# Optimization experiments

Measured on AMD Instinct MI355X. Metric: run time of the kernel, lower is better.

The kernel has to match this reference:

```python
import jax, jax.numpy as jnp
import numpy as np


def conv2d(x, w, pad):
    # x: [N,C,H,W], w: [O,I,kh,kw]
    return jax.lax.conv_general_dilated(
        x, w, window_strides=(1, 1), padding=[(pad, pad), (pad, pad)],
        dimension_numbers=("NCHW", "OIHW", "NCHW"))


def group_norm1(x, g, b, eps=1e-5):
    # GroupNorm(1, C): normalize over (C,H,W) per sample, per-channel affine
    mu = jnp.mean(x, axis=(1, 2, 3), keepdims=True)
    var = jnp.mean((x - mu) ** 2, axis=(1, 2, 3), keepdims=True)
    xn = (x - mu) * jax.lax.rsqrt(var + eps)
    return xn * g[None, :, None, None] + b[None, :, None, None]


def maxpool_3x3_s2(x):
    return jax.lax.reduce_window(
        x, -jnp.inf, jax.lax.max, (1, 1, 3, 3), (1, 1, 2, 2),
        ((0, 0), (0, 0), (1, 1), (1, 1)))


def hr2o_layer(x, wq, wk, wv, wo, g, b):
    # x: [N,C,H,W]; pairwise attention over the N ROIs at each (h,w)
    q = conv2d(x, wq, 1)
    k = conv2d(x, wk, 1)
    v = conv2d(x, wv, 1)
    scale = 1.0 / jnp.sqrt(jnp.asarray(x.shape[1], x.dtype))
    # torch: (q.unsqueeze(1) * k.unsqueeze(0)).sum(2) == einsum over channels
    att = jnp.einsum("nchw,mchw->nmhw", q, k) * scale  # [N,N,H,W]
    att = jax.nn.softmax(att, axis=1)                    # softmax over keys (dim=1)
    virt = jnp.einsum("nmhw,mchw->nchw", att, v)        # [N,C,H,W]
    virt = jax.nn.relu(group_norm1(virt, g, b))
    virt = conv2d(virt, wo, 1)
    return x + virt  # dropout is identity in eval mode


def setup_inputs() -> dict:
    key = jax.random.key(0)
    ks = jax.random.split(key, 12)
    N, C_R, H, W, HID, NCLS, DEPTH = 64, 1024, 16, 16, 512, 60, 2
    s = 0.02
    return {
        "bg_feats": jax.random.normal(ks[0], (C_R, H, W), jnp.float32),
        "actor_feats": jax.random.normal(ks[1], (N, C_R), jnp.float32),
        "w_conv1": jax.random.normal(ks[2], (HID, 2 * C_R, 1, 1), jnp.float32) * s,
        "w_conv2": jax.random.normal(ks[3], (HID, HID, 3, 3), jnp.float32) * s,
        "w_q": jax.random.normal(ks[4], (DEPTH, HID, HID, 3, 3), jnp.float32) * s,
        "w_k": jax.random.normal(ks[5], (DEPTH, HID, HID, 3, 3), jnp.float32) * s,
        "w_v": jax.random.normal(ks[6], (DEPTH, HID, HID, 3, 3), jnp.float32) * s,
        "w_o": jax.random.normal(ks[7], (DEPTH, HID, HID, 3, 3), jnp.float32) * s,
        "gamma": jnp.ones((DEPTH, HID), jnp.float32),
        "beta": jnp.zeros((DEPTH, HID), jnp.float32),
        "w_fc1": jax.random.normal(ks[8], (HID, C_R), jnp.float32) * s,
        "w_fc2": jax.random.normal(ks[9], (NCLS, 2 * HID), jnp.float32) * s,
    }


def reference(bg_feats, actor_feats, w_conv1, w_conv2, w_q, w_k, w_v, w_o,
              gamma, beta, w_fc1, w_fc2):
    N = actor_feats.shape[0]
    C_R, H, W = bg_feats.shape
    # bg repeated per ROI, actor features tiled over spatial dims
    bg = jnp.broadcast_to(bg_feats[None], (N, C_R, H, W))
    tiled = jnp.broadcast_to(actor_feats[:, :, None, None], (N, C_R, H, W))
    x = jnp.concatenate([bg, tiled], axis=1)           # [N, 2*C_R, H, W]
    x = jax.nn.relu(conv2d(x, w_conv1, 0))             # 1x1 -> [N,HID,H,W]
    x = jax.nn.relu(conv2d(x, w_conv2, 0))             # 3x3 pad=0 -> H-2,W-2
    x = maxpool_3x3_s2(x)                              # -> 7x7
    for d in range(w_q.shape[0]):
        x = hr2o_layer(x, w_q[d], w_k[d], w_v[d], w_o[d], gamma[d], beta[d])
    high_order = jnp.mean(x, axis=(2, 3))              # gap -> [N,HID]
    roi = jax.nn.relu(actor_feats @ w_fc1.T)           # [N,HID]
    out = jnp.concatenate([roi, high_order], axis=1) @ w_fc2.T  # [N,num_classes]
    return out
```

## Files before the change

### kernel.cpp

```cpp
#include <hip/hip_runtime.h>
#include <math.h>


typedef __bf16 bf16x8 __attribute__((ext_vector_type(8)));
typedef float  f32x4  __attribute__((ext_vector_type(4)));

#define NROI 64
#define CR   1024
#define HIDC 512
#define NCLS 60
#define PLANE (NROI * HIDC * 49)
#define ROWH 40
#define OCALL 4608
#define TAPSTR ((size_t)OCALL * 512)
#define WL (HIDC * HIDC * 9)
#define GNCNT 25088.0f

#if defined(__has_builtin)
#  if __has_builtin(__builtin_amdgcn_global_load_lds)
#    define HAVE_GLL 1
#  endif
#endif

__device__ __forceinline__ void stage16(const void* g, void* lds_base, int lane) {
#ifdef HAVE_GLL
    __builtin_amdgcn_global_load_lds(
        (const __attribute__((address_space(1))) unsigned int*)g,
        (__attribute__((address_space(3))) unsigned int*)lds_base, 16, 0, 0);
#else
    *(uint4*)((char*)lds_base + lane * 16) = *(const uint4*)g;
#endif
}

__device__ __forceinline__ float bf2f(unsigned short h) {
    union { unsigned u; float f; } x; x.u = (unsigned)h << 16; return x.f;
}

__device__ __forceinline__ unsigned short f2bfu(float f) {
    return __builtin_bit_cast(unsigned short, (__bf16)f);
}

__device__ __forceinline__ int swzkey(int r) {
    return (r & 3) ^ ((r >> 2) & 3);
}

__global__ __launch_bounds__(256) void k_mega(
    const float* __restrict__ bg, const float* __restrict__ actor,
    const float* __restrict__ w1, const float* __restrict__ wfc1,
    const float* __restrict__ w2, const float* __restrict__ wq,
    const float* __restrict__ wk, const float* __restrict__ wv,
    const float* __restrict__ wo,
    float* __restrict__ A_T, float* __restrict__ Bp, float* __restrict__ roi,
    __bf16* __restrict__ wAll, __bf16* __restrict__ inT7)
{
    const int b = blockIdx.x, tid = threadIdx.x;
    __shared__ __align__(16) char smem[18432];

    if (b < 48) {
        const int bx = b % 6, by = b / 6;
        const bool isA = bx < 4;
        const bool isRoi = (bx == 5);
        const int ocWg = by * 64;
        const int w = tid >> 6, lane = tid & 63;
        const int q = lane >> 4, l16 = lane & 15;
        __bf16* s_a = (__bf16*)smem;
        __bf16* s_b = s_a + 64 * ROWH;

        f32x4 acc[4];
#pragma unroll
        for (int nt = 0; nt < 4; ++nt) acc[nt] = (f32x4){0.f, 0.f, 0.f, 0.f};

        const int row = tid >> 2, part = tid & 3;
        for (int ch = 0; ch < 32; ++ch) {
            const int c0 = ch * 32;
            __syncthreads();
            if (isA) {
                const int gp = bx * 64 + row;
                bf16x8 val;
#pragma unroll
                for (int j = 0; j < 8; ++j)
                    val[j] = (__bf16)bg[(size_t)(c0 + part * 8 + j) * 256 + gp];
                *(bf16x8*)(&s_a[row * ROWH + part * 8]) = val;
            } else {
                const float* src = actor + (size_t)row * CR + c0 + part * 8;
                bf16x8 val;
#pragma unroll
                for (int j = 0; j < 8; ++j) val[j] = (__bf16)src[j];
                *(bf16x8*)(&s_a[row * ROWH + part * 8]) = val;
            }
            {
                const float* srcb = isRoi
                    ? (wfc1 + (size_t)(ocWg + row) * CR + c0 + part * 8)
                    : (w1 + (size_t)(ocWg + row) * (2 * CR)
                          + (isA ? 0 : CR) + c0 + part * 8);
                bf16x8 vb;
#pragma unroll
                for (int j = 0; j < 8; ++j) vb[j] = (__bf16)srcb[j];
                *(bf16x8*)(&s_b[row * ROWH + part * 8]) = vb;
            }
            __syncthreads();
            const bf16x8 af = *(const bf16x8*)(&s_a[(w * 16 + l16) * ROWH + q * 8]);
#pragma unroll
            for (int nt = 0; nt < 4; ++nt) {
                const bf16x8 bw = *(const bf16x8*)(&s_b[(nt * 16 + l16) * ROWH + q * 8]);
                acc[nt] = __builtin_amdgcn_mfma_f32_16x16x32_bf16(af, bw, acc[nt], 0, 0, 0);
            }
        }
#pragma unroll
        for (int r = 0; r < 4; ++r) {
#pragma unroll
            for (int nt = 0; nt < 4; ++nt) {
                const int mrow = w * 16 + q * 4 + r;
                const int oc = ocWg + nt * 16 + l16;
                if (isA)       A_T[(size_t)(bx * 64 + mrow) * 512 + oc] = acc[nt][r];
                else if (isRoi) roi[(size_t)mrow * 512 + oc] = fmaxf(acc[nt][r], 0.f);
                else           Bp[(size_t)mrow * 512 + oc] = acc[nt][r];
            }
        }
    } else if (b < 4656) {
        const int bid = b - 48;
        const float* src;
        if (bid < 512) src = w2 + (size_t)bid * 4608;
        else if (bid < 2048) {
            const int r = bid - 512;
            const float* bb = r < 512 ? wq : (r < 1024 ? wk : wv);
            src = bb + (size_t)(r & 511) * 4608;
        } else if (bid < 2560) src = wo + (size_t)(bid - 2048) * 4608;
        else if (bid < 4096) {
            const int r = bid - 2560;
            const float* bb = r < 512 ? wq : (r < 1024 ? wk : wv);
            src = bb + WL + (size_t)(r & 511) * 4608;
        } else src = wo + WL + (size_t)(bid - 4096) * 4608;
        float* s = (float*)smem;
        const float4* s4 = (const float4*)src;
        for (int i = tid; i < 1152; i += 256) ((float4*)s)[i] = s4[i];
        __syncthreads();
        for (int u = tid; u < 576; u += 256) {
            const int t = u / 64, o = u - (u / 64) * 64;
            const int swz = (o & 3) ^ ((bid >> 1) & 3);
            const int cbase = o * 8;
            unsigned pack[4];
#pragma unroll
            for (int h = 0; h < 4; ++h) {
                const unsigned short lo = f2bfu(s[(cbase + 2 * h) * 9 + t]);
                const unsigned short hi = f2bfu(s[(cbase + 2 * h + 1) * 9 + t]);
                pack[h] = ((unsigned)hi << 16) | lo;
            }
            const size_t cidx = (size_t)(o >> 2) * 32 + (size_t)swz * 8;
            *(uint4*)(wAll + (size_t)t * TAPSTR + (size_t)bid * 512 + cidx) =
                *(const uint4*)pack;
        }
    } else {
        const int k = b - 4656;
        const int n = k >> 3;
        const int j0 = (k & 7) * 4;
#pragma unroll
        for (int i = 0; i < 4; ++i) {
            const int jj = j0 + i;
            int sp;
            if (jj < 9) sp = jj;
            else if (jj < 18) sp = 63 + jj;
            else { const int t = jj - 18; sp = (1 + (t >> 1)) * 9 + (t & 1) * 8; }
            unsigned* d = (unsigned*)(inT7 + ((size_t)n * 81 + sp) * 512);
            d[tid] = 0u;
        }
    }
}

__global__ __launch_bounds__(256) void k_prep_in2(
    const float* __restrict__ A_T, const float* __restrict__ B,
    __bf16* __restrict__ dst)
{
    const int vn = blockIdx.x;
    const int n = vn >> 2, quad = vn & 3;
    const int sp0 = blockIdx.y * 27;
    const float b0 = B[n * HIDC + threadIdx.x];
    const float b1 = B[n * HIDC + 256 + threadIdx.x];
    for (int sp = sp0; sp < sp0 + 27; ++sp) {
        const int r = sp / 9, w = sp % 9;
        const int p16 = ((quad >> 1) * 7 + r) * 16 + (quad & 1) * 7 + w;
        __bf16* d = dst + ((size_t)vn * 81 + sp) * 512;
        d[threadIdx.x]       = (__bf16)fmaxf(A_T[p16 * HIDC + threadIdx.x] + b0, 0.f);
        d[256 + threadIdx.x] = (__bf16)fmaxf(A_T[p16 * HIDC + 256 + threadIdx.x] + b1, 0.f);
    }
}

__global__ __launch_bounds__(256) void k_prep_gn(
    const float* __restrict__ virt, const float* __restrict__ statsRaw,
    const float* __restrict__ gamma, const float* __restrict__ beta,
    __bf16* __restrict__ gnT)
{
    const int vn = blockIdx.x;
    const int sp0 = blockIdx.y * 9;
    __shared__ float s_mi[2];
    if (threadIdx.x == 0) {
        const float S = statsRaw[vn * 2], Q = statsRaw[vn * 2 + 1];
        const float mean = S / GNCNT;
        s_mi[0] = mean;
        s_mi[1] = rsqrtf(Q / GNCNT - mean * mean + 1e-5f);
    }
    __syncthreads();
    const float m = s_mi[0], iv = s_mi[1];
    const int c0 = threadIdx.x, c1 = threadIdx.x + 256;
    const float g0 = gamma[c0], g1 = gamma[c1];
    const float b0 = beta[c0],  b1 = beta[c1];
    for (int sp = sp0; sp < sp0 + 9; ++sp) {
        const int rr = sp / 9, cc = sp % 9;
        __bf16* d = gnT + ((size_t)vn * 81 + sp) * 512;
        if (rr >= 1 && rr <= 7 && cc >= 1 && cc <= 7) {
            const int p = (rr - 1) * 7 + (cc - 1);
            const float* src = virt + ((size_t)vn * 49 + p) * 512;
            d[c0] = (__bf16)fmaxf((src[c0] - m) * iv * g0 + b0, 0.f);
            d[c1] = (__bf16)fmaxf((src[c1] - m) * iv * g1 + b1, 0.f);
        } else {
            d[c0] = (__bf16)0.f;
            d[c1] = (__bf16)0.f;
        }
    }
}

template<int VN, int MODE, int OCT>
__global__ __launch_bounds__(256, (VN == 4) ? 2 : 3) void k_conv_pipe(
    const __bf16* __restrict__ inT,
    const __bf16* __restrict__ wAll, int ocBaseGl,
    __bf16* __restrict__ outb,
    float* __restrict__ zeroStats, float* __restrict__ gapZero,
    const float* __restrict__ resid, float* __restrict__ outf,
    __bf16* __restrict__ inT7out, float* __restrict__ gapOut)
{
    constexpr int MT = (VN == 4) ? 4 : 2;
    constexpr int SLOTS = VN * 324;
    constexpr int NSUB = (SLOTS + 255) / 256;
    constexpr int SBUF = NSUB * 256;
    constexpr int NI = NSUB / 3;
    constexpr int WTAP = OCT * 512;
    constexpr int SWSZ = 2 * 3 * WTAP + ((OCT == 2) ? 1024 : 0);
    const int tid = threadIdx.x;
    const int w = tid >> 6, lane = tid & 63;
    const int q = lane >> 4, l16 = lane & 15;
    const int vn_l = (VN == 4) ? w : (w & 1);
    const int mh   = (VN == 4) ? 0 : (w >> 1);
    const int vnBase = blockIdx.x * VN;
    const int ocWg = blockIdx.y * (OCT * 16);

    if (zeroStats && blockIdx.x == 0 && blockIdx.y == 0 && tid < 128)
        zeroStats[tid] = 0.f;
    if (gapZero && blockIdx.y == 0 && blockIdx.x < 16) {
        const float4 z = {0.f, 0.f, 0.f, 0.f};
        ((float4*)gapZero)[blockIdx.x * 512 + tid * 2]     = z;
        ((float4*)gapZero)[blockIdx.x * 512 + tid * 2 + 1] = z;
    }

    __shared__ __align__(16) __bf16 s_w[SWSZ];
    __shared__ __align__(16) __bf16 s_in[2 * SBUF * 8];

    unsigned iGo[NSUB];
#pragma unroll
    for (int s = 0; s < NSUB; ++s) {
        int idx = tid + s * 256;
        if (idx > SLOTS - 1) idx = SLOTS - 1;
        const int vnl = idx / 324, rem = idx - vnl * 324;
        const int r = rem >> 2, part = rem & 3;
        iGo[s] = (unsigned)(((vnBase + vnl) * 81 + r) * 512
                            + ((part ^ swzkey(r)) * 8));
    }
    unsigned wGo4 = 0;
    unsigned wGo2[2]; int wJ2[2];
    if constexpr (OCT == 4) {
        wGo4 = (unsigned)((ocBaseGl + ocWg + (tid >> 2)) * 512 + (tid & 3) * 8);
    } else {
#pragma unroll
        for (int k = 0; k < 2; ++k) {
            const int u = tid + k * 256;
            const int jj = (u >> 7) > 2 ? 2 : (u >> 7);
            const int row = (u >> 2) & 31, part = u & 3;
            wGo2[k] = (unsigned)((ocBaseGl + ocWg + row) * 512 + part * 8);
            wJ2[k] = jj;
        }
    }
    const int bOff = l16 * 32 + ((q ^ ((l16 >> 1) & 3)) << 3);

    int aLoc[MT];
#pragma unroll
    for (int mt = 0; mt < MT; ++mt) {
        int p = (mh * MT + mt) * 16 + l16;
        p = p > 48 ? 48 : p;
        aLoc[mt] = (p / 7) * 9 + (p % 7);
    }
    const int vb81 = vn_l * 81;

    f32x4 acc[MT][OCT];
#pragma unroll
    for (int a = 0; a < MT; ++a)
#pragma unroll
        for (int b = 0; b < OCT; ++b) acc[a][b] = (f32x4){0.f, 0.f, 0.f, 0.f};

    auto stageW = [&](int fn, int cc, int wparN) {
        if constexpr (OCT == 4) {
#pragma unroll
            for (int j = 0; j < 3; ++j)
                stage16(wAll + (size_t)(fn * 3 + j) * TAPSTR + wGo4 + cc,
                        (char*)s_w + (size_t)(wparN * 3 + j) * (WTAP * 2)
                                    + (size_t)w * 1024, lane);
        } else {
#pragma unroll
            for (int k = 0; k < 2; ++k) {
                const int ubase = (tid & ~63) + k * 256;
                char* dst;
                if (ubase < 384)
                    dst = (char*)s_w
                        + (size_t)(wparN * 3 + (ubase >> 7)) * (WTAP * 2)
                        + (size_t)(ubase & 127) * 16;
                else
                    dst = (char*)s_w + (size_t)(2 * 3 * WTAP) * 2
                        + (size_t)(ubase - 384) * 16;
                stage16(wAll + (size_t)(fn * 3 + wJ2[k]) * TAPSTR + wGo2[k] + cc,
                        dst, lane);
            }
        }
    };

#pragma unroll
    for (int s = 0; s < NSUB; ++s)
        stage16(inT + iGo[s],
                (char*)s_in + (size_t)(s * 256 + w * 64) * 16, lane);
    stageW(0, 0, 0);
    __syncthreads();

    for (int ch = 0; ch < 16; ++ch) {
        const int c0 = ch * 32;
        const int cur = ch & 1;
        const int nxt = cur ^ 1;
#pragma unroll
        for (int f = 0; f < 3; ++f) {
            const int P = ch * 3 + f;
            const int wpar = P & 1;
            {
                const int fn = (f == 2) ? 0 : (f + 1);
                const int cc = (f == 2) ? (c0 + 32) : c0;
                stageW(fn, cc, wpar ^ 1);
            }
#pragma unroll
            for (int u = 0; u < NI; ++u) {
                const int s = f * NI + u;
                stage16(inT + iGo[s] + c0 + 32,
                        (char*)s_in + (size_t)nxt * (SBUF * 16)
                                    + (size_t)(s * 256 + w * 64) * 16, lane);
            }
            if (f == 0) {
                if constexpr (OCT == 4) {
                    if constexpr (NI == 2) asm volatile("s_waitcnt vmcnt(5)" ::: "memory");
                    else                   asm volatile("s_waitcnt vmcnt(4)" ::: "memory");
                } else {
                    asm volatile("s_waitcnt vmcnt(3)" ::: "memory");
                }
            } else {
                if constexpr (OCT == 4) {
                    if constexpr (NI == 2) asm volatile("s_waitcnt vmcnt(7)" ::: "memory");
                    else                   asm volatile("s_waitcnt vmcnt(5)" ::: "memory");
                } else {
                    asm volatile("s_waitcnt vmcnt(4)" ::: "memory");
                }
            }
            __builtin_amdgcn_sched_barrier(0);
            __builtin_amdgcn_s_barrier();
            __builtin_amdgcn_sched_barrier(0);
#pragma unroll
            for (int j = 0; j < 3; ++j) {
                const int DT = f * 9 + j;
                bf16x8 bw[OCT];
#pragma unroll
                for (int nt = 0; nt < OCT; ++nt)
                    bw[nt] = *(const bf16x8*)(
                        &s_w[(wpar * 3 + j) * WTAP + nt * 512 + bOff]);
                bf16x8 af[MT];
#pragma unroll
                for (int mt = 0; mt < MT; ++mt) {
                    const int rl = aLoc[mt] + DT;
                    const int col = (q ^ swzkey(rl)) << 3;
                    af[mt] = *(const bf16x8*)(
                        &s_in[cur * (SBUF * 8) + (vb81 + rl) * 32 + col]);
                }
#pragma unroll
                for (int mt = 0; mt < MT; ++mt)
#pragma unroll
                    for (int nt = 0; nt < OCT; ++nt)
                        acc[mt][nt] = __builtin_amdgcn_mfma_f32_16x16x32_bf16(
                            af[mt], bw[nt], acc[mt][nt], 0, 0, 0);
            }
            __builtin_amdgcn_sched_barrier(0);
            __builtin_amdgcn_s_barrier();
        }
    }

    const int vn = vnBase + vn_l;
    float gsum[OCT];
#pragma unroll
    for (int nt = 0; nt < OCT; ++nt) gsum[nt] = 0.f;
#pragma unroll
    for (int mt = 0; mt < MT; ++mt) {
#pragma unroll
        for (int r = 0; r < 4; ++r) {
            const int p = (mh * MT + mt) * 16 + q * 4 + r;
            if (p >= 49) continue;
#pragma unroll
            for (int nt = 0; nt < OCT; ++nt) {
                const int oc = ocWg + nt * 16 + l16;
                const float v = acc[mt][nt][r];
                if constexpr (MODE == 2) {
                    const int n = vn >> 2, quad = vn & 3;
                    const int p14 = ((quad >> 1) * 7 + p / 7) * 14 + (quad & 1) * 7 + p % 7;
                    outb[((size_t)n * 196 + p14) * 512 + oc] = (__bf16)fmaxf(v, 0.f);
                } else if constexpr (MODE == 1) {
                    const size_t addr = ((size_t)vn * 49 + p) * 512 + oc;
                    const float res = v + resid[addr];
                    if (!gapOut) outf[addr] = res;
                    gsum[nt] += res;
                    if (inT7out) {
                        const int sp = (p / 7 + 1) * 9 + (p % 7 + 1);
                        inT7out[((size_t)vn * 81 + sp) * 512 + oc] = (__bf16)res;
                    }
                } else {
                    const int conv = oc >> 9;
                    outb[(size_t)conv * PLANE + ((size_t)p * 64 + vn) * 512 + (oc & 511)]
                        = (__bf16)v;
                }
            }
        }
    }
    if constexpr (MODE == 1) {
        if (gapOut) {
#pragma unroll
            for (int nt = 0; nt < OCT; ++nt)
                atomicAdd(gapOut + (size_t)vn * 512 + ocWg + nt * 16 + l16, gsum[nt]);
        }
    }
}

__global__ __launch_bounds__(256) void k_pool_prep(
    const __bf16* __restrict__ x2, __bf16* __restrict__ inT7,
    float* __restrict__ xA)
{
    const int b = blockIdx.x;
    const int n = b / 49, p = b % 49;
    const int i = p / 7, j = p % 7;
    const int sp = (i + 1) * 9 + (j + 1);
#pragma unroll
    for (int k = 0; k < 2; ++k) {
        const int c = threadIdx.x + k * 256;
        float mx = -1e30f;
#pragma unroll
        for (int di = -1; di <= 1; ++di) {
            const int rr = 2 * i + di;
            if (rr < 0 || rr >= 14) continue;
#pragma unroll
            for (int dj = -1; dj <= 1; ++dj) {
                const int cc = 2 * j + dj;
                if (cc < 0 || cc >= 14) continue;
                mx = fmaxf(mx, (float)x2[((size_t)n * 196 + rr * 14 + cc) * 512 + c]);
            }
        }
        inT7[((size_t)n * 81 + sp) * 512 + c] = (__bf16)mx;
        xA[((size_t)n * 49 + p) * 512 + c] = mx;
    }
}

__global__ __launch_bounds__(256) void k_attvirt(
    const __bf16* __restrict__ qT, const __bf16* __restrict__ kT,
    const __bf16* __restrict__ vT, float* __restrict__ virt,
    float* __restrict__ statsRaw)
{
    const int p = blockIdx.y;
    const int w = threadIdx.x >> 6, m = threadIdx.x & 63;
    const int n = blockIdx.x * 4 + w;
    __shared__ float s_q[4][HIDC];
    __shared__ float s_a[4][64];
    {
        const uint4 v = ((const uint4*)(qT + ((size_t)p * 64 + n) * HIDC))[m];
        const unsigned* u = (const unsigned*)&v;
#pragma unroll
        for (int j = 0; j < 4; ++j) {
            s_q[w][m * 8 + 2 * j]     = bf2f((unsigned short)(u[j] & 0xffff));
            s_q[w][m * 8 + 2 * j + 1] = bf2f((unsigned short)(u[j] >> 16));
        }
    }
    __syncthreads();
    const uint4* krow = (const uint4*)(kT + ((size_t)p * 64 + m) * HIDC);
    float acc0 = 0.f, acc1 = 0.f;
    for (int i = 0; i < 64; ++i) {
        const uint4 v = krow[i];
        const unsigned* u = (const unsigned*)&v;
#pragma unroll
        for (int j = 0; j < 2; ++j) {
            acc0 = fmaf(s_q[w][i * 8 + 2 * j],     bf2f((unsigned short)(u[j] & 0xffff)), acc0);
            acc0 = fmaf(s_q[w][i * 8 + 2 * j + 1], bf2f((unsigned short)(u[j] >> 16)),    acc0);
        }
#pragma unroll
        for (int j = 2; j < 4; ++j) {
            acc1 = fmaf(s_q[w][i * 8 + 2 * j],     bf2f((unsigned short)(u[j] & 0xffff)), acc1);
            acc1 = fmaf(s_q[w][i * 8 + 2 * j + 1], bf2f((unsigned short)(u[j] >> 16)),    acc1);
        }
    }
    float acc = (acc0 + acc1) * 0.044194173824159216f;
    float mx = acc;
#pragma unroll
    for (int off = 32; off; off >>= 1) mx = fmaxf(mx, __shfl_xor(mx, off));
    const float e = expf(acc - mx);
    float s = e;
#pragma unroll
    for (int off = 32; off; off >>= 1) s += __shfl_xor(s, off);
    s_a[w][m] = e / s;
    __syncthreads();
    const int c0 = m * 8;
    float av[8];
#pragma unroll
    for (int j = 0; j < 8; ++j) av[j] = 0.f;
    for (int mm = 0; mm < 64; ++mm) {
        const float a = s_a[w][mm];
        const uint4 v = *(const uint4*)(vT + ((size_t)p * 64 + mm) * HIDC + c0);
        const unsigned* u = (const unsigned*)&v;
#pragma unroll
        for (int j = 0; j < 4; ++j) {
            av[2 * j]     = fmaf(a, bf2f((unsigned short)(u[j] & 0xffff)), av[2 * j]);
            av[2 * j + 1] = fmaf(a, bf2f((unsigned short)(u[j] >> 16)),    av[2 * j + 1]);
        }
    }
    float* o = virt + ((size_t)n * 49 + p) * 512 + c0;
    float ps = 0.f, pq = 0.f;
#pragma unroll
    for (int j = 0; j < 8; ++j) {
        o[j] = av[j];
        ps += av[j];
        pq = fmaf(av[j], av[j], pq);
    }
#pragma unroll
    for (int off = 32; off; off >>= 1) {
        ps += __shfl_xor(ps, off);
        pq += __shfl_xor(pq, off);
    }
    if (m == 0) {
        atomicAdd(statsRaw + n * 2, ps);
        atomicAdd(statsRaw + n * 2 + 1, pq);
    }
}

__global__ __launch_bounds__(256) void k_final(
    const float* __restrict__ roi, const float* __restrict__ gap,
    const float* __restrict__ wfc2, float* __restrict__ out)
{
    const int n = blockIdx.x, tid = threadIdx.x;
    __shared__ float s[1024];
    s[tid]       = roi[(size_t)n * 512 + tid];
    s[tid + 256] = roi[(size_t)n * 512 + 256 + tid];
    s[tid + 512] = gap[(size_t)n * 512 + tid] * (1.f / 49.f);
    s[tid + 768] = gap[(size_t)n * 512 + 256 + tid] * (1.f / 49.f);
    __syncthreads();
    if (tid < 240) {
        const int k = tid >> 2, part = tid & 3;
        const float4* w4 = (const float4*)(wfc2 + (size_t)k * 1024 + part * 256);
        const float4* s4 = (const float4*)(s + part * 256);
        float a0 = 0.f, a1 = 0.f, a2 = 0.f, a3 = 0.f;
        for (int i = 0; i < 64; ++i) {
            const float4 wv = w4[i], sv = s4[i];
            a0 = fmaf(wv.x, sv.x, a0); a1 = fmaf(wv.y, sv.y, a1);
            a2 = fmaf(wv.z, sv.z, a2); a3 = fmaf(wv.w, sv.w, a3);
        }
        float acc = (a0 + a1) + (a2 + a3);
        acc += __shfl_xor(acc, 1);
        acc += __shfl_xor(acc, 2);
        if (part == 0) out[n * NCLS + k] = acc;
    }
}

extern "C" void kernel_launch(void* const* d_in, const int* in_sizes, int n_in,
                              void* d_out, int out_size, void* d_ws, size_t ws_size,
                              hipStream_t stream) {
    const float* bg    = (const float*)d_in[0];
    const float* actor = (const float*)d_in[1];
    const float* w1    = (const float*)d_in[2];
    const float* w2    = (const float*)d_in[3];
    const float* wq    = (const float*)d_in[4];
    const float* wk    = (const float*)d_in[5];
    const float* wv    = (const float*)d_in[6];
    const float* wo    = (const float*)d_in[7];
    const float* gamma = (const float*)d_in[8];
    const float* beta  = (const float*)d_in[9];
    const float* wfc1  = (const float*)d_in[10];
    const float* wfc2  = (const float*)d_in[11];
    float* out = (float*)d_out;
    float* ws  = (float*)d_ws;

    float* A_T   = ws;
    float* Bp    = A_T + 131072;
    float* xA    = Bp + 32768;
    float* xB    = xA + PLANE;
    float* stats = xB + PLANE;
    float* roi   = stats + 128;
    float* gap   = roi + 32768;
    float* fend  = gap + 32768;
    __bf16* x2h  = (__bf16*)fend;
    float*  virt = (float*)x2h;
    __bf16* inT2 = x2h + 6422528;
    __bf16* qkvT = inT2;
    __bf16* inT7 = inT2 + 10616832;
    __bf16* wAll = inT7 + 2654208;
    __bf16* gnT  = wAll + (size_t)9 * OCALL * 512 + 262144;

    k_mega<<<5168, 256, 0, stream>>>(bg, actor, w1, wfc1, w2, wq, wk, wv, wo,
                                     A_T, Bp, roi, wAll, inT7);
    k_prep_in2<<<dim3(256, 3), 256, 0, stream>>>(A_T, Bp, inT2);
    k_conv_pipe<4, 2, 4><<<dim3(64, 8), 256, 0, stream>>>(
        inT2, wAll, 0, x2h, nullptr, nullptr,
        nullptr, nullptr, nullptr, nullptr);
    k_pool_prep<<<64 * 49, 256, 0, stream>>>(x2h, inT7, xA);

    float* xin = xA;
    float* xout = xB;
    for (int d = 0; d < 2; ++d) {
        k_conv_pipe<2, 0, 4><<<dim3(32, 24), 256, 0, stream>>>(
            inT7, wAll, 512 + d * 2048, qkvT, stats,
            d == 1 ? gap : nullptr,
            nullptr, nullptr, nullptr, nullptr);
        k_attvirt<<<dim3(16, 49), 256, 0, stream>>>(
            qkvT, qkvT + PLANE, qkvT + 2 * PLANE, virt, stats);
        k_prep_gn<<<dim3(64, 9), 256, 0, stream>>>(
            virt, stats, gamma + d * HIDC, beta + d * HIDC, gnT);
        k_conv_pipe<2, 1, 2><<<dim3(32, 16), 256, 0, stream>>>(
            gnT, wAll, 2048 + d * 2048, nullptr, nullptr, nullptr,
            xin, xout, d == 0 ? inT7 : nullptr, d == 1 ? gap : nullptr);
        float* t = xin; xin = xout; xout = t;
    }
    k_final<<<64, 256, 0, stream>>>(roi, gap, wfc2, out);
}
```

Before: 571.3 us.

## Fuse GroupNorm prep into attention kernel via last-block completion counter

Removes the separate k_prep_gn launch. Each k_attvirt block increments a per-ROI atomic counter, and the last of the 49 position blocks for an ROI applies GroupNorm, ReLU and bf16 conversion into the padded gnT buffer. The zero border of gnT is now written once in k_mega instead of on every call. The counters are reset through the existing stats-zeroing path. This saves a launch and a pass over global memory, but the final block per ROI does a serial 49-position loop, which risks a tail at the end of the kernel.

```diff
diff --git a/kernel.cpp b/kernel.cpp
--- a/kernel.cpp
+++ b/kernel.cpp
@@ -51,7 +51,8 @@
     const float* __restrict__ wk, const float* __restrict__ wv,
     const float* __restrict__ wo,
     float* __restrict__ A_T, float* __restrict__ Bp, float* __restrict__ roi,
-    __bf16* __restrict__ wAll, __bf16* __restrict__ inT7)
+    __bf16* __restrict__ wAll, __bf16* __restrict__ inT7,
+    __bf16* __restrict__ gnT)
 {
     const int b = blockIdx.x, tid = threadIdx.x;
     __shared__ __align__(16) char smem[18432];
@@ -151,7 +152,8 @@
                 *(const uint4*)pack;
         }
     } else {
-        const int k = b - 4656;
+        const int k = (b < 5168) ? (b - 4656) : (b - 5168);
+        __bf16* base = (b < 5168) ? inT7 : gnT;
         const int n = k >> 3;
         const int j0 = (k & 7) * 4;
 #pragma unroll
@@ -161,7 +163,7 @@
             if (jj < 9) sp = jj;
             else if (jj < 18) sp = 63 + jj;
             else { const int t = jj - 18; sp = (1 + (t >> 1)) * 9 + (t & 1) * 8; }
-            unsigned* d = (unsigned*)(inT7 + ((size_t)n * 81 + sp) * 512);
+            unsigned* d = (unsigned*)(base + ((size_t)n * 81 + sp) * 512);
             d[tid] = 0u;
         }
     }
@@ -182,40 +184,6 @@
         __bf16* d = dst + ((size_t)vn * 81 + sp) * 512;
         d[threadIdx.x]       = (__bf16)fmaxf(A_T[p16 * HIDC + threadIdx.x] + b0, 0.f);
         d[256 + threadIdx.x] = (__bf16)fmaxf(A_T[p16 * HIDC + 256 + threadIdx.x] + b1, 0.f);
-    }
-}
-
-__global__ __launch_bounds__(256) void k_prep_gn(
-    const float* __restrict__ virt, const float* __restrict__ statsRaw,
-    const float* __restrict__ gamma, const float* __restrict__ beta,
-    __bf16* __restrict__ gnT)
-{
-    const int vn = blockIdx.x;
-    const int sp0 = blockIdx.y * 9;
-    __shared__ float s_mi[2];
-    if (threadIdx.x == 0) {
-        const float S = statsRaw[vn * 2], Q = statsRaw[vn * 2 + 1];
-        const float mean = S / GNCNT;
-        s_mi[0] = mean;
-        s_mi[1] = rsqrtf(Q / GNCNT - mean * mean + 1e-5f);
-    }
-    __syncthreads();
-    const float m = s_mi[0], iv = s_mi[1];
-    const int c0 = threadIdx.x, c1 = threadIdx.x + 256;
-    const float g0 = gamma[c0], g1 = gamma[c1];
-    const float b0 = beta[c0],  b1 = beta[c1];
-    for (int sp = sp0; sp < sp0 + 9; ++sp) {
-        const int rr = sp / 9, cc = sp % 9;
-        __bf16* d = gnT + ((size_t)vn * 81 + sp) * 512;
-        if (rr >= 1 && rr <= 7 && cc >= 1 && cc <= 7) {
-            const int p = (rr - 1) * 7 + (cc - 1);
-            const float* src = virt + ((size_t)vn * 49 + p) * 512;
-            d[c0] = (__bf16)fmaxf((src[c0] - m) * iv * g0 + b0, 0.f);
-            d[c1] = (__bf16)fmaxf((src[c1] - m) * iv * g1 + b1, 0.f);
-        } else {
-            d[c0] = (__bf16)0.f;
-            d[c1] = (__bf16)0.f;
-        }
     }
 }
 
@@ -243,7 +211,7 @@
     const int vnBase = blockIdx.x * VN;
     const int ocWg = blockIdx.y * (OCT * 16);
 
-    if (zeroStats && blockIdx.x == 0 && blockIdx.y == 0 && tid < 128)
+    if (zeroStats && blockIdx.x == 0 && blockIdx.y == 0 && tid < 192)
         zeroStats[tid] = 0.f;
     if (gapZero && blockIdx.y == 0 && blockIdx.x < 16) {
         const float4 z = {0.f, 0.f, 0.f, 0.f};
@@ -468,13 +436,16 @@
 __global__ __launch_bounds__(256) void k_attvirt(
     const __bf16* __restrict__ qT, const __bf16* __restrict__ kT,
     const __bf16* __restrict__ vT, float* __restrict__ virt,
-    float* __restrict__ statsRaw)
+    float* __restrict__ statsRaw, int* __restrict__ cnt,
+    const float* __restrict__ gamma, const float* __restrict__ beta,
+    __bf16* __restrict__ gnT)
 {
     const int p = blockIdx.y;
     const int w = threadIdx.x >> 6, m = threadIdx.x & 63;
     const int n = blockIdx.x * 4 + w;
     __shared__ float s_q[4][HIDC];
     __shared__ float s_a[4][64];
+    __shared__ int s_flag[4];
     {
         const uint4 v = ((const uint4*)(qT + ((size_t)p * 64 + n) * HIDC))[m];
         const unsigned* u = (const unsigned*)&v;
@@ -541,6 +512,34 @@
     if (m == 0) {
         atomicAdd(statsRaw + n * 2, ps);
         atomicAdd(statsRaw + n * 2 + 1, pq);
+    }
+
+    __threadfence();
+    __syncthreads();
+    if (m == 0) {
+        const int prev = atomicAdd(cnt + n, 1);
+        s_flag[w] = (prev == 48) ? 1 : 0;
+    }
+    __syncthreads();
+#pragma unroll
+    for (int nn = 0; nn < 4; ++nn) {
+        if (s_flag[nn]) {
+            __threadfence();
+            const int gn = blockIdx.x * 4 + nn;
+            const float S = statsRaw[gn * 2], Q = statsRaw[gn * 2 + 1];
+            const float mean = S / GNCNT;
+            const float iv = rsqrtf(Q / GNCNT - mean * mean + 1e-5f);
+            const int ca = threadIdx.x, cb = threadIdx.x + 256;
+            const float g0 = gamma[ca], g1 = gamma[cb];
+            const float b0 = beta[ca],  b1 = beta[cb];
+            for (int pp = 0; pp < 49; ++pp) {
+                const float* src = virt + ((size_t)gn * 49 + pp) * 512;
+                __bf16* dpt = gnT + ((size_t)gn * 81
+                                     + (pp / 7 + 1) * 9 + (pp % 7 + 1)) * 512;
+                dpt[ca] = (__bf16)fmaxf((src[ca] - mean) * iv * g0 + b0, 0.f);
+                dpt[cb] = (__bf16)fmaxf((src[cb] - mean) * iv * g1 + b1, 0.f);
+            }
+        }
     }
 }
 
@@ -595,7 +594,8 @@
     float* xA    = Bp + 32768;
     float* xB    = xA + PLANE;
     float* stats = xB + PLANE;
-    float* roi   = stats + 128;
+    int*   cnt   = (int*)(stats + 128);
+    float* roi   = stats + 192;
     float* gap   = roi + 32768;
     float* fend  = gap + 32768;
     __bf16* x2h  = (__bf16*)fend;
@@ -606,8 +606,8 @@
     __bf16* wAll = inT7 + 2654208;
     __bf16* gnT  = wAll + (size_t)9 * OCALL * 512 + 262144;
 
-    k_mega<<<5168, 256, 0, stream>>>(bg, actor, w1, wfc1, w2, wq, wk, wv, wo,
-                                     A_T, Bp, roi, wAll, inT7);
+    k_mega<<<5680, 256, 0, stream>>>(bg, actor, w1, wfc1, w2, wq, wk, wv, wo,
+                                     A_T, Bp, roi, wAll, inT7, gnT);
     k_prep_in2<<<dim3(256, 3), 256, 0, stream>>>(A_T, Bp, inT2);
     k_conv_pipe<4, 2, 4><<<dim3(64, 8), 256, 0, stream>>>(
         inT2, wAll, 0, x2h, nullptr, nullptr,
@@ -622,9 +622,8 @@
             d == 1 ? gap : nullptr,
             nullptr, nullptr, nullptr, nullptr);
         k_attvirt<<<dim3(16, 49), 256, 0, stream>>>(
-            qkvT, qkvT + PLANE, qkvT + 2 * PLANE, virt, stats);
-        k_prep_gn<<<dim3(64, 9), 256, 0, stream>>>(
-            virt, stats, gamma + d * HIDC, beta + d * HIDC, gnT);
+            qkvT, qkvT + PLANE, qkvT + 2 * PLANE, virt, stats, cnt,
+            gamma + d * HIDC, beta + d * HIDC, gnT);
         k_conv_pipe<2, 1, 2><<<dim3(32, 16), 256, 0, stream>>>(
             gnT, wAll, 2048 + d * 2048, nullptr, nullptr, nullptr,
             xin, xout, d == 0 ? inT7 : nullptr, d == 1 ? gap : nullptr);
```

New measurement: 832.6 us. +45.7%, slower.
